# Performance work log

Hardware: AMD Instinct MI355X
Metric: run time of the kernel (lower is better)

## Reference

```python
import jax, jax.numpy as jnp
import numpy as np

SPATIAL_SCALE = 0.0625
GAMMA = 0.1  # mmcv DeformRoIPool default
NUM_HEADS = 1


def deform_roi_pool(features, rois, offsets, spatial_scale=SPATIAL_SCALE, gamma=GAMMA):
    """mmcv-style deformable RoI (align) pooling, sampling_ratio=1.
    features: (B,C,H,W); rois: (N,5)=[b,x1,y1,x2,y2]; offsets: (P,oh,ow,2) (dw,dh).
    Returns (P,N,C,oh,ow)."""
    B, C, H, W = features.shape
    N = rois.shape[0]
    P, oh, ow, _ = offsets.shape
    bidx = rois[:, 0].astype(jnp.int32)
    x1 = rois[:, 1] * spatial_scale - 0.5
    y1 = rois[:, 2] * spatial_scale - 0.5
    rw = rois[:, 3] * spatial_scale - 0.5 - x1
    rh = rois[:, 4] * spatial_scale - 0.5 - y1
    bin_w = rw / ow
    bin_h = rh / oh
    gh = jnp.arange(oh, dtype=features.dtype)
    gw = jnp.arange(ow, dtype=features.dtype)
    # bin-center sample points (sampling_ratio=1), deformed by gamma*roi_size*offset
    y = (y1[:, None, None] + (gh[None, :, None] + 0.5) * bin_h[:, None, None])[None]
    y = y + gamma * rh[None, :, None, None] * offsets[:, None, :, :, 1]  # (P,N,oh,ow)
    x = (x1[:, None, None] + (gw[None, None, :] + 0.5) * bin_w[:, None, None])[None]
    x = x + gamma * rw[None, :, None, None] * offsets[:, None, :, :, 0]
    valid = (y > -1.0) & (y < H) & (x > -1.0) & (x < W)
    yc = jnp.clip(y, 0.0, H - 1)
    xc = jnp.clip(x, 0.0, W - 1)
    y0 = jnp.floor(yc).astype(jnp.int32)
    x0 = jnp.floor(xc).astype(jnp.int32)
    y1i = jnp.minimum(y0 + 1, H - 1)
    x1i = jnp.minimum(x0 + 1, W - 1)
    ly = yc - y0.astype(yc.dtype)
    lx = xc - x0.astype(xc.dtype)
    hy = 1.0 - ly
    hx = 1.0 - lx
    f = features.reshape(B, C, H * W)
    bb = jnp.broadcast_to(bidx[None, :, None, None], (P, N, oh, ow))

    def g(yi, xi):
        return f[bb, :, yi * W + xi]  # (P,N,oh,ow,C)

    val = (g(y0, x0) * (hy * hx)[..., None] + g(y0, x1i) * (hy * lx)[..., None]
           + g(y1i, x0) * (ly * hx)[..., None] + g(y1i, x1i) * (ly * lx)[..., None])
    val = jnp.where(valid[..., None], val, 0.0)
    return jnp.transpose(val, (0, 1, 4, 2, 3))  # (P,N,C,oh,ow)


def setup_inputs() -> dict:
    key = jax.random.key(0)
    ks = jax.random.split(key, 9)
    B, C, Hf, Wf = 4, 256, 128, 128
    N, oh, ow, P = 512, 7, 7, 4
    features = jax.random.normal(ks[0], (B, C, Hf, Wf), jnp.float32)
    bidx = jax.random.randint(ks[1], (N,), 0, B).astype(jnp.float32)
    xy1 = jax.random.uniform(ks[2], (N, 2), jnp.float32, 0.0, 1700.0)
    wh = jax.random.uniform(ks[3], (N, 2), jnp.float32, 32.0, 300.0)
    rois = jnp.concatenate([bidx[:, None], xy1, xy1 + wh], axis=1)  # (N,5)
    per_point_offsets = jax.random.normal(ks[4], (P, oh, ow, 2), jnp.float32) * 0.001
    queries = jax.random.normal(ks[5], (oh * ow, C), jnp.float32) * 0.02
    w_proj = jax.random.normal(ks[6], (C, C), jnp.float32) * 0.02
    b_proj = jnp.zeros((C,), jnp.float32)
    in_proj_w = jax.random.normal(ks[7], (3 * C, C), jnp.float32) * 0.02
    in_proj_b = jnp.zeros((3 * C,), jnp.float32)
    out_proj_w = jax.random.normal(ks[8], (C, C), jnp.float32) * 0.02
    out_proj_b = jnp.zeros((C,), jnp.float32)
    return dict(features=features, rois=rois, per_point_offsets=per_point_offsets,
                queries=queries, w_proj=w_proj, b_proj=b_proj,
                in_proj_w=in_proj_w, in_proj_b=in_proj_b,
                out_proj_w=out_proj_w, out_proj_b=out_proj_b)


def reference(features, rois, per_point_offsets, queries, w_proj, b_proj,
              in_proj_w, in_proj_b, out_proj_w, out_proj_b):
    samples = deform_roi_pool(features, rois, per_point_offsets)  # (P,N,C,oh,ow)
    P, N, C, oh, ow = samples.shape
    # 1x1 conv projection
    proj = jnp.einsum('pnchw,dc->pndhw', samples, w_proj) + b_proj[None, None, :, None, None]
    kv = jnp.transpose(proj, (0, 1, 3, 4, 2)).reshape(P, N * oh * ow, C)  # (P,B,C)
    q = jnp.tile(queries, (N, 1))  # (B,C), B=(n,h,w) order
    Wq, Wk, Wv = in_proj_w[:C], in_proj_w[C:2 * C], in_proj_w[2 * C:]
    bq, bk, bv = in_proj_b[:C], in_proj_b[C:2 * C], in_proj_b[2 * C:]
    H = NUM_HEADS
    d = C // H
    Q = (q @ Wq.T + bq).reshape(-1, H, d)
    K = (kv @ Wk.T + bk).reshape(P, -1, H, d)
    V = (kv @ Wv.T + bv).reshape(P, -1, H, d)
    scores = jnp.einsum('bhd,pbhd->bhp', Q, K) * (d ** -0.5)
    attn = jax.nn.softmax(scores, axis=-1)  # over the P sampled points
    out = jnp.einsum('bhp,pbhd->bhd', attn, V).reshape(-1, C)
    out = out @ out_proj_w.T + out_proj_b
    return out.reshape(N, oh, ow, C).transpose(0, 3, 1, 2)  # (N,C,oh,ow)
```

## Files before the change

kernel.cpp:

```cpp
#include <hip/hip_runtime.h>
#include <math.h>

#define C_DIM 256
#define H_DIM 128
#define W_DIM 128
#define B_DIM 4
#define HW (H_DIM*W_DIM)
#define N_ROIS 512
#define OH 7
#define OW 7
#define TOKENS (N_ROIS*OH*OW)
#define SPS 0.0625f
#define GAMMA 0.1f
#define SCALE 0.0625f

typedef __attribute__((ext_vector_type(8))) short bf16x8;
typedef __attribute__((ext_vector_type(4))) float f32x4;
typedef __attribute__((ext_vector_type(4))) unsigned short us4;
typedef __attribute__((ext_vector_type(8))) unsigned short us8;

__device__ inline unsigned short f2bf_rne(float f) {
    unsigned int b = __float_as_uint(f);
    b += 0x7fffu + ((b >> 16) & 1u);
    return (unsigned short)(b >> 16);
}
__device__ inline float bfu(unsigned short u) {
    return __uint_as_float(((unsigned int)u) << 16);
}

__global__ void precompute1(const float* __restrict__ w_proj,
                            const float* __restrict__ in_proj_w,
                            const float* __restrict__ in_proj_b,
                            const float* __restrict__ queries,
                            const float* __restrict__ b_proj,
                            float* __restrict__ A_k, float* __restrict__ A_v,
                            float* __restrict__ Qhat, float* __restrict__ cv) {
    int idx = blockIdx.x * 256 + threadIdx.x;
    if (idx < 65536) {
        int i = idx >> 8, j = idx & 255;
        const float* wk = in_proj_w + (size_t)(256 + i) * 256;
        float s = 0.f;
        for (int t = 0; t < 256; t++) s += wk[t] * w_proj[t * 256 + j];
        A_k[idx] = s;
    } else if (idx < 131072) {
        int e = idx - 65536;
        int i = e >> 8, j = e & 255;
        const float* wv = in_proj_w + (size_t)(512 + i) * 256;
        float s = 0.f;
        for (int t = 0; t < 256; t++) s += wv[t] * w_proj[t * 256 + j];
        A_v[e] = s;
    } else if (idx < 143616) {
        int e = idx - 131072;
        int s_ = e >> 8, i = e & 255;
        const float* q  = queries + (size_t)s_ * 256;
        const float* wq = in_proj_w + (size_t)i * 256;
        float s = in_proj_b[i];
        for (int t = 0; t < 256; t++) s += q[t] * wq[t];
        Qhat[e] = s;
    } else {
        int i = idx - 143616;
        const float* wv = in_proj_w + (size_t)(512 + i) * 256;
        float s = in_proj_b[512 + i];
        for (int t = 0; t < 256; t++) s += wv[t] * b_proj[t];
        cv[i] = s;
    }
}

__global__ void precompute2(const float* __restrict__ Qhat,
                            const float* __restrict__ A_k,
                            const float* __restrict__ A_v,
                            const float* __restrict__ out_proj_w,
                            const float* __restrict__ out_proj_b,
                            const float* __restrict__ cv,
                            float* __restrict__ u,
                            unsigned short* __restrict__ Mh,
                            unsigned short* __restrict__ Ml,
                            float* __restrict__ Mtp, int writeMtp,
                            float* __restrict__ c_out) {
    int idx = blockIdx.x * 256 + threadIdx.x;
    if (idx < 12544) {
        int s_ = idx >> 8, j = idx & 255;
        const float* qh = Qhat + (size_t)s_ * 256;
        float s = 0.f;
        for (int i = 0; i < 256; i++) s += qh[i] * A_k[i * 256 + j];
        u[idx] = s;
    } else if (idx < 78080) {
        int e = idx - 12544;
        int c = e >> 8, d = e & 255;
        const float* wo = out_proj_w + (size_t)c * 256;
        float s = 0.f;
        for (int i = 0; i < 256; i++) s += wo[i] * A_v[i * 256 + d];
        unsigned short hi = f2bf_rne(s);
        float fh = bfu(hi);
        unsigned short lo = f2bf_rne(s - fh);
        Mh[(size_t)c * 256 + d] = hi;
        Ml[(size_t)c * 256 + d] = lo;
        if (writeMtp)
            Mtp[((size_t)(d >> 2) * 256 + c) * 4 + (d & 3)] = s;
    } else {
        int c = idx - 78080;
        const float* wo = out_proj_w + (size_t)c * 256;
        float s = out_proj_b[c];
        for (int i = 0; i < 256; i++) s += wo[i] * cv[i];
        c_out[c] = s;
    }
}

__global__ void transpose_bf16(const float* __restrict__ f,
                               unsigned short* __restrict__ ft) {
    __shared__ float tile[64][65];
    int b  = blockIdx.z;
    int c0 = blockIdx.y * 64;
    int s0 = blockIdx.x * 64;
    const float* fin = f + (size_t)b * C_DIM * HW;
    int sl = threadIdx.x & 63, cw = threadIdx.x >> 6;
    #pragma unroll
    for (int k = 0; k < 16; k++) {
        int cl = cw + k * 4;
        tile[cl][sl] = fin[(size_t)(c0 + cl) * HW + s0 + sl];
    }
    __syncthreads();
    unsigned short* fo = ft + (size_t)b * HW * C_DIM;
    int cl = threadIdx.x & 63, sw = threadIdx.x >> 6;
    #pragma unroll
    for (int k = 0; k < 16; k++) {
        int sl2 = sw + k * 4;
        fo[(size_t)(s0 + sl2) * C_DIM + c0 + cl] = f2bf_rne(tile[cl][sl2]);
    }
}

__global__ void __launch_bounds__(256) fused_sample_gemm(
        const unsigned short* __restrict__ feat_b,
        const float* __restrict__ rois,
        const float* __restrict__ offs,
        const float* __restrict__ u,
        const unsigned short* __restrict__ Mh,
        const unsigned short* __restrict__ Ml,
        const float* __restrict__ c_out,
        float* __restrict__ out) {
    __shared__ __align__(16) char ldsraw[54272];
    unsigned short* A = (unsigned short*)ldsraw;

    int tid = threadIdx.x;
    int n = blockIdx.x;

    const float* r = rois + (size_t)n * 5;
    int bi   = (int)r[0];
    float x1 = r[1] * SPS - 0.5f;
    float y1v = r[2] * SPS - 0.5f;
    float rw = r[3] * SPS - 0.5f - x1;
    float rh = r[4] * SPS - 0.5f - y1v;
    float bw = rw * (1.0f / 7.0f);
    float bh = rh * (1.0f / 7.0f);
    const unsigned short* fb = feat_b + (size_t)bi * HW * C_DIM;

    int lane32 = tid & 31;
    int halfw  = tid >> 5;
    int c8 = lane32 * 8;

    for (int t = halfw; t < 49; t += 8) {
        int hb = t / 7, wb = t - hb * 7;
        const float* up = u + (size_t)t * 256 + c8;
        float uu[8];
        *(float4*)uu       = *(const float4*)up;
        *(float4*)(uu + 4) = *(const float4*)(up + 4);

        float sv[4][8];
        float part[4];
        #pragma unroll
        for (int p = 0; p < 4; p++) {
            float offw = offs[((p * 7 + hb) * 7 + wb) * 2 + 0];
            float offh = offs[((p * 7 + hb) * 7 + wb) * 2 + 1];
            float y = y1v + ((float)hb + 0.5f) * bh + GAMMA * rh * offh;
            float x = x1  + ((float)wb + 0.5f) * bw + GAMMA * rw * offw;
            bool valid = (y > -1.0f) && (y < 128.0f) && (x > -1.0f) && (x < 128.0f);
            float yc = fminf(fmaxf(y, 0.f), 127.f);
            float xc = fminf(fmaxf(x, 0.f), 127.f);
            int y0i = (int)yc, x0i = (int)xc;
            int y1i = min(y0i + 1, 127), x1i = min(x0i + 1, 127);
            float ly = yc - (float)y0i, lx = xc - (float)x0i;
            float hy = 1.f - ly, hx = 1.f - lx;
            float w00 = hy * hx, w01 = hy * lx, w10 = ly * hx, w11 = ly * lx;
            if (!valid) { w00 = 0.f; w01 = 0.f; w10 = 0.f; w11 = 0.f; }
            us8 r00 = *(const us8*)(fb + (size_t)(y0i * W_DIM + x0i) * C_DIM + c8);
            us8 r01 = *(const us8*)(fb + (size_t)(y0i * W_DIM + x1i) * C_DIM + c8);
            us8 r10 = *(const us8*)(fb + (size_t)(y1i * W_DIM + x0i) * C_DIM + c8);
            us8 r11 = *(const us8*)(fb + (size_t)(y1i * W_DIM + x1i) * C_DIM + c8);
            float accp = 0.f;
            #pragma unroll
            for (int j = 0; j < 8; j++) {
                float v = w00 * bfu(r00[j]) + w01 * bfu(r01[j])
                        + w10 * bfu(r10[j]) + w11 * bfu(r11[j]);
                sv[p][j] = v;
                accp = fmaf(uu[j], v, accp);
            }
            part[p] = accp;
        }
        #pragma unroll
        for (int mk = 1; mk <= 16; mk <<= 1) {
            #pragma unroll
            for (int p = 0; p < 4; p++) part[p] += __shfl_xor(part[p], mk, 64);
        }
        float sc0 = part[0] * SCALE, sc1 = part[1] * SCALE;
        float sc2 = part[2] * SCALE, sc3 = part[3] * SCALE;
        float mx = fmaxf(fmaxf(sc0, sc1), fmaxf(sc2, sc3));
        float e0 = __expf(sc0 - mx), e1 = __expf(sc1 - mx);
        float e2 = __expf(sc2 - mx), e3 = __expf(sc3 - mx);
        float inv = 1.f / (e0 + e1 + e2 + e3);
        us8 o8;
        #pragma unroll
        for (int j = 0; j < 8; j++) {
            float mv = (e0 * sv[0][j] + e1 * sv[1][j]
                      + e2 * sv[2][j] + e3 * sv[3][j]) * inv;
            o8[j] = f2bf_rne(mv);
        }
        *(us8*)(A + t * 264 + c8) = o8;
    }
    for (int i = tid; i < 480; i += 256) {
        int row = 49 + (i >> 5);
        int cs = (i & 31) * 8;
        us8 z = {0, 0, 0, 0, 0, 0, 0, 0};
        *(us8*)(A + row * 264 + cs) = z;
    }
    __syncthreads();

    int lane = tid & 63;
    int wave = tid >> 6;
    int col  = lane & 15;
    int quad = lane >> 4;
    int cbase = wave * 64;

    f32x4 zero = {0.f, 0.f, 0.f, 0.f};
    f32x4 acc[4][4];
    #pragma unroll
    for (int i = 0; i < 4; i++)
        #pragma unroll
        for (int j = 0; j < 4; j++) acc[i][j] = zero;

    for (int ks = 0; ks < 8; ks++) {
        bf16x8 af[4];
        #pragma unroll
        for (int rt = 0; rt < 4; rt++)
            af[rt] = *(const bf16x8*)(A + (rt * 16 + col) * 264 + ks * 32 + quad * 8);
        #pragma unroll
        for (int ct = 0; ct < 4; ct++) {
            size_t bo = (size_t)(cbase + ct * 16 + col) * 256 + ks * 32 + quad * 8;
            bf16x8 bh8 = *(const bf16x8*)(Mh + bo);
            bf16x8 bl8 = *(const bf16x8*)(Ml + bo);
            #pragma unroll
            for (int rt = 0; rt < 4; rt++) {
                acc[rt][ct] = __builtin_amdgcn_mfma_f32_16x16x32_bf16(af[rt], bh8, acc[rt][ct], 0, 0, 0);
                acc[rt][ct] = __builtin_amdgcn_mfma_f32_16x16x32_bf16(af[rt], bl8, acc[rt][ct], 0, 0, 0);
            }
        }
    }

    __syncthreads();
    float* ostage = (float*)ldsraw;
    #pragma unroll
    for (int rt = 0; rt < 4; rt++) {
        #pragma unroll
        for (int ct = 0; ct < 4; ct++) {
            int c = cbase + ct * 16 + col;
            float bias = c_out[c];
            #pragma unroll
            for (int rr = 0; rr < 4; rr++) {
                int t = rt * 16 + quad * 4 + rr;
                if (t < 49) ostage[c * 53 + t] = acc[rt][ct][rr] + bias;
            }
        }
    }
    __syncthreads();
    float* ob = out + (size_t)n * 12544;
    for (int k = 0; k < 49; k++) {
        int flat = k * 256 + tid;
        int c2 = flat / 49;
        int t2 = flat - c2 * 49;
        ob[flat] = ostage[c2 * 53 + t2];
    }
}

__global__ void sample_generic(const float* __restrict__ feat,
                               const float* __restrict__ rois,
                               const float* __restrict__ offs,
                               const float* __restrict__ u,
                               float* __restrict__ m_out,
                               int ch_stride, int pix_stride) {
    __shared__ float red[4][4];
    int token = blockIdx.x;
    int n = token / 49;
    int t = token - n * 49;
    int h = t / 7;
    int w = t - h * 7;
    const float* r = rois + (size_t)n * 5;
    int bi   = (int)r[0];
    float x1 = r[1] * SPS - 0.5f;
    float y1 = r[2] * SPS - 0.5f;
    float rw = r[3] * SPS - 0.5f - x1;
    float rh = r[4] * SPS - 0.5f - y1;
    float bw = rw * (1.0f / 7.0f);
    float bh = rh * (1.0f / 7.0f);
    int c = threadIdx.x;
    const float* fb = feat + (size_t)bi * HW * C_DIM;
    float u_c = u[(size_t)t * 256 + c];
    float sv[4], part[4];
    #pragma unroll
    for (int p = 0; p < 4; p++) {
        float offw = offs[((p * 7 + h) * 7 + w) * 2 + 0];
        float offh = offs[((p * 7 + h) * 7 + w) * 2 + 1];
        float y = y1 + ((float)h + 0.5f) * bh + GAMMA * rh * offh;
        float x = x1 + ((float)w + 0.5f) * bw + GAMMA * rw * offw;
        bool valid = (y > -1.0f) && (y < (float)H_DIM) && (x > -1.0f) && (x < (float)W_DIM);
        float yc = fminf(fmaxf(y, 0.f), 127.f);
        float xc = fminf(fmaxf(x, 0.f), 127.f);
        int y0i = (int)floorf(yc);
        int x0i = (int)floorf(xc);
        int y1i = min(y0i + 1, 127);
        int x1i = min(x0i + 1, 127);
        float ly = yc - (float)y0i, lx = xc - (float)x0i;
        float hy = 1.f - ly, hx = 1.f - lx;
        float v00 = fb[(size_t)(y0i * W_DIM + x0i) * pix_stride + (size_t)c * ch_stride];
        float v01 = fb[(size_t)(y0i * W_DIM + x1i) * pix_stride + (size_t)c * ch_stride];
        float v10 = fb[(size_t)(y1i * W_DIM + x0i) * pix_stride + (size_t)c * ch_stride];
        float v11 = fb[(size_t)(y1i * W_DIM + x1i) * pix_stride + (size_t)c * ch_stride];
        float v = hy * hx * v00 + hy * lx * v01 + ly * hx * v10 + ly * lx * v11;
        v = valid ? v : 0.f;
        sv[p] = v;
        part[p] = u_c * v;
    }
    #pragma unroll
    for (int o = 32; o >= 1; o >>= 1) {
        #pragma unroll
        for (int p = 0; p < 4; p++) part[p] += __shfl_down(part[p], o, 64);
    }
    int wv = threadIdx.x >> 6, lane = threadIdx.x & 63;
    if (lane == 0) {
        red[wv][0] = part[0]; red[wv][1] = part[1];
        red[wv][2] = part[2]; red[wv][3] = part[3];
    }
    __syncthreads();
    float sc0 = (red[0][0] + red[1][0] + red[2][0] + red[3][0]) * SCALE;
    float sc1 = (red[0][1] + red[1][1] + red[2][1] + red[3][1]) * SCALE;
    float sc2 = (red[0][2] + red[1][2] + red[2][2] + red[3][2]) * SCALE;
    float sc3 = (red[0][3] + red[1][3] + red[2][3] + red[3][3]) * SCALE;
    float mx = fmaxf(fmaxf(sc0, sc1), fmaxf(sc2, sc3));
    float e0 = __expf(sc0 - mx), e1 = __expf(sc1 - mx);
    float e2 = __expf(sc2 - mx), e3 = __expf(sc3 - mx);
    float inv = 1.f / (e0 + e1 + e2 + e3);
    m_out[(size_t)token * 256 + c] =
        (e0 * sv[0] + e1 * sv[1] + e2 * sv[2] + e3 * sv[3]) * inv;
}

__global__ void __launch_bounds__(256) roi_gemm(const float* __restrict__ m,
                                                const float* __restrict__ Mtp,
                                                const float* __restrict__ c_out,
                                                float* __restrict__ out) {
    __shared__ float mlds[49 * 260];
    int c = threadIdx.x;
    int n = blockIdx.x;
    const float* mb = m + (size_t)n * 12544;
    for (int t = 0; t < 49; t++) mlds[t * 260 + c] = mb[t * 256 + c];
    __syncthreads();
    float acc[49];
    #pragma unroll
    for (int t = 0; t < 49; t++) acc[t] = 0.f;
    const float4* Mp = (const float4*)Mtp;
    for (int d4 = 0; d4 < 64; d4++) {
        float4 w4 = Mp[(size_t)d4 * 256 + c];
        #pragma unroll
        for (int t = 0; t < 49; t++) {
            float4 mv = *(const float4*)&mlds[t * 260 + d4 * 4];
            acc[t] = fmaf(w4.x, mv.x, acc[t]);
            acc[t] = fmaf(w4.y, mv.y, acc[t]);
            acc[t] = fmaf(w4.z, mv.z, acc[t]);
            acc[t] = fmaf(w4.w, mv.w, acc[t]);
        }
    }
    float bias = c_out[c];
    __syncthreads();
    #pragma unroll
    for (int t = 0; t < 49; t++) mlds[t * 260 + c] = acc[t] + bias;
    __syncthreads();
    float* ob = out + (size_t)n * 12544;
    for (int k = 0; k < 49; k++) {
        int flat = k * 256 + c;
        int c2 = flat / 49;
        int t2 = flat - c2 * 49;
        ob[flat] = mlds[t2 * 260 + c2];
    }
}

extern "C" void kernel_launch(void* const* d_in, const int* in_sizes, int n_in,
                              void* d_out, int out_size, void* d_ws, size_t ws_size,
                              hipStream_t stream) {
    (void)in_sizes; (void)n_in; (void)out_size;
    const float* features   = (const float*)d_in[0];
    const float* rois       = (const float*)d_in[1];
    const float* offs       = (const float*)d_in[2];
    const float* queries    = (const float*)d_in[3];
    const float* w_proj     = (const float*)d_in[4];
    const float* b_proj     = (const float*)d_in[5];
    const float* in_proj_w  = (const float*)d_in[6];
    const float* in_proj_b  = (const float*)d_in[7];
    const float* out_proj_w = (const float*)d_in[8];
    const float* out_proj_b = (const float*)d_in[9];
    float* out = (float*)d_out;
    float* ws  = (float*)d_ws;

    float* A_k   = ws;
    float* A_v   = A_k  + 65536;
    float* Qhat  = A_v  + 65536;
    float* cv    = Qhat + 12544;
    float* u     = cv   + 256;
    float* c_out = u    + 12544;
    unsigned short* Mh = (unsigned short*)(ws + 156672);
    unsigned short* Ml = (unsigned short*)(ws + 189440);
    unsigned short* feat_b = (unsigned short*)(ws + 222208);
    float* Mtp    = ws + 222208;
    float* m_fb   = ws + 222208 + 65536;

    size_t needT = ((size_t)222208 + (size_t)8388608) * 4;
    size_t needF = ((size_t)222208 + (size_t)65536 + (size_t)TOKENS * 256) * 4;
    bool useT = ws_size >= needT;

    precompute1<<<562, 256, 0, stream>>>(w_proj, in_proj_w, in_proj_b,
                                         queries, b_proj, A_k, A_v, Qhat, cv);
    precompute2<<<306, 256, 0, stream>>>(Qhat, A_k, A_v, out_proj_w, out_proj_b,
                                         cv, u, Mh, Ml, Mtp, useT ? 0 : 1, c_out);

    if (useT) {
        transpose_bf16<<<dim3(256, 4, 4), 256, 0, stream>>>(features, feat_b);
        fused_sample_gemm<<<N_ROIS, 256, 0, stream>>>(feat_b, rois, offs, u,
                                                      Mh, Ml, c_out, out);
    } else {
        float* m = (ws_size >= needF) ? m_fb : out;
        sample_generic<<<TOKENS, 256, 0, stream>>>(features, rois, offs, u, m, HW, 1);
        roi_gemm<<<512, 256, 0, stream>>>(m, Mtp, c_out, out);
    }
}
```

Before: 180.8 us.

## Fuse precompute, transpose and sampling GEMM into one cooperative persistent kernel

Merges the two weight-precompute kernels, the feature transpose and the fused sample+GEMM kernel into a single cooperative kernel with 512 blocks, using grid.sync between phases. Precompute1 runs alongside the transpose, and precompute2 follows after the first grid barrier. This removes three kernel launch gaps and the tail idle time between them, at the cost of two grid-wide barriers and an occupancy check on the host. The fallback path also replaces the fp32 roi_gemm with a bf16 hi/lo MFMA version, and falls back to separate launches if the cooperative launch fails.

```diff
diff --git a/kernel.cpp b/kernel.cpp
--- a/kernel.cpp
+++ b/kernel.cpp
@@ -1,22 +1,21 @@
 #include <hip/hip_runtime.h>
+#include <hip/hip_cooperative_groups.h>
 #include <math.h>
+
+namespace cg = cooperative_groups;
 
 #define C_DIM 256
 #define H_DIM 128
 #define W_DIM 128
-#define B_DIM 4
 #define HW (H_DIM*W_DIM)
 #define N_ROIS 512
-#define OH 7
-#define OW 7
-#define TOKENS (N_ROIS*OH*OW)
+#define TOKENS (N_ROIS*49)
 #define SPS 0.0625f
 #define GAMMA 0.1f
 #define SCALE 0.0625f
 
 typedef __attribute__((ext_vector_type(8))) short bf16x8;
 typedef __attribute__((ext_vector_type(4))) float f32x4;
-typedef __attribute__((ext_vector_type(4))) unsigned short us4;
 typedef __attribute__((ext_vector_type(8))) unsigned short us8;
 
 __device__ inline unsigned short f2bf_rne(float f) {
@@ -28,14 +27,12 @@
     return __uint_as_float(((unsigned int)u) << 16);
 }
 
-__global__ void precompute1(const float* __restrict__ w_proj,
-                            const float* __restrict__ in_proj_w,
-                            const float* __restrict__ in_proj_b,
-                            const float* __restrict__ queries,
-                            const float* __restrict__ b_proj,
-                            float* __restrict__ A_k, float* __restrict__ A_v,
-                            float* __restrict__ Qhat, float* __restrict__ cv) {
-    int idx = blockIdx.x * 256 + threadIdx.x;
+
+__device__ inline void dev_pre1(int idx,
+                                const float* w_proj, const float* in_proj_w,
+                                const float* in_proj_b, const float* queries,
+                                const float* b_proj,
+                                float* A_k, float* A_v, float* Qhat, float* cv) {
     if (idx < 65536) {
         int i = idx >> 8, j = idx & 255;
         const float* wk = in_proj_w + (size_t)(256 + i) * 256;
@@ -57,7 +54,7 @@
         float s = in_proj_b[i];
         for (int t = 0; t < 256; t++) s += q[t] * wq[t];
         Qhat[e] = s;
-    } else {
+    } else if (idx < 143872) {
         int i = idx - 143616;
         const float* wv = in_proj_w + (size_t)(512 + i) * 256;
         float s = in_proj_b[512 + i];
@@ -66,18 +63,12 @@
     }
 }
 
-__global__ void precompute2(const float* __restrict__ Qhat,
-                            const float* __restrict__ A_k,
-                            const float* __restrict__ A_v,
-                            const float* __restrict__ out_proj_w,
-                            const float* __restrict__ out_proj_b,
-                            const float* __restrict__ cv,
-                            float* __restrict__ u,
-                            unsigned short* __restrict__ Mh,
-                            unsigned short* __restrict__ Ml,
-                            float* __restrict__ Mtp, int writeMtp,
-                            float* __restrict__ c_out) {
-    int idx = blockIdx.x * 256 + threadIdx.x;
+__device__ inline void dev_pre2(int idx,
+                                const float* Qhat, const float* A_k, const float* A_v,
+                                const float* out_proj_w, const float* out_proj_b,
+                                const float* cv,
+                                float* u, unsigned short* Mh, unsigned short* Ml,
+                                float* c_out) {
     if (idx < 12544) {
         int s_ = idx >> 8, j = idx & 255;
         const float* qh = Qhat + (size_t)s_ * 256;
@@ -91,13 +82,10 @@
         float s = 0.f;
         for (int i = 0; i < 256; i++) s += wo[i] * A_v[i * 256 + d];
         unsigned short hi = f2bf_rne(s);
-        float fh = bfu(hi);
-        unsigned short lo = f2bf_rne(s - fh);
+        unsigned short lo = f2bf_rne(s - bfu(hi));
         Mh[(size_t)c * 256 + d] = hi;
         Ml[(size_t)c * 256 + d] = lo;
-        if (writeMtp)
-            Mtp[((size_t)(d >> 2) * 256 + c) * 4 + (d & 3)] = s;
-    } else {
+    } else if (idx < 78336) {
         int c = idx - 78080;
         const float* wo = out_proj_w + (size_t)c * 256;
         float s = out_proj_b[c];
@@ -106,52 +94,48 @@
     }
 }
 
-__global__ void transpose_bf16(const float* __restrict__ f,
-                               unsigned short* __restrict__ ft) {
-    __shared__ float tile[64][65];
-    int b  = blockIdx.z;
-    int c0 = blockIdx.y * 64;
-    int s0 = blockIdx.x * 64;
-    const float* fin = f + (size_t)b * C_DIM * HW;
-    int sl = threadIdx.x & 63, cw = threadIdx.x >> 6;
-    #pragma unroll
-    for (int k = 0; k < 16; k++) {
-        int cl = cw + k * 4;
+__device__ inline void dev_transpose_tile(char* ldsraw, int tile_id, int tid,
+                                          const float* features,
+                                          unsigned short* feat_b) {
+    float (*tile)[65] = (float (*)[65])ldsraw;
+    int b   = tile_id >> 10;
+    int rem = tile_id & 1023;
+    int c0  = (rem >> 8) << 6;
+    int s0  = (rem & 255) << 6;
+    int sl = tid & 63, cw = tid >> 6;
+    const float* fin = features + (size_t)b * C_DIM * HW;
+    #pragma unroll
+    for (int kk = 0; kk < 16; kk++) {
+        int cl = cw + kk * 4;
         tile[cl][sl] = fin[(size_t)(c0 + cl) * HW + s0 + sl];
     }
     __syncthreads();
-    unsigned short* fo = ft + (size_t)b * HW * C_DIM;
-    int cl = threadIdx.x & 63, sw = threadIdx.x >> 6;
-    #pragma unroll
-    for (int k = 0; k < 16; k++) {
-        int sl2 = sw + k * 4;
-        fo[(size_t)(s0 + sl2) * C_DIM + c0 + cl] = f2bf_rne(tile[cl][sl2]);
-    }
-}
-
-__global__ void __launch_bounds__(256) fused_sample_gemm(
-        const unsigned short* __restrict__ feat_b,
-        const float* __restrict__ rois,
-        const float* __restrict__ offs,
-        const float* __restrict__ u,
-        const unsigned short* __restrict__ Mh,
-        const unsigned short* __restrict__ Ml,
-        const float* __restrict__ c_out,
-        float* __restrict__ out) {
-    __shared__ __align__(16) char ldsraw[54272];
+    unsigned short* fo = feat_b + (size_t)b * HW * C_DIM;
+    #pragma unroll
+    for (int kk = 0; kk < 16; kk++) {
+        int sl2 = cw + kk * 4;
+        fo[(size_t)(s0 + sl2) * C_DIM + c0 + sl] = f2bf_rne(tile[sl][sl2]);
+    }
+    __syncthreads();
+}
+
+__device__ inline void dev_sample_gemm(char* ldsraw, int n, int tid,
+                                       const unsigned short* feat_b,
+                                       const float* rois, const float* offs,
+                                       const float* u,
+                                       const unsigned short* Mh,
+                                       const unsigned short* Ml,
+                                       const float* c_out, float* out) {
     unsigned short* A = (unsigned short*)ldsraw;
 
-    int tid = threadIdx.x;
-    int n = blockIdx.x;
-
     const float* r = rois + (size_t)n * 5;
-    int bi   = (int)r[0];
-    float x1 = r[1] * SPS - 0.5f;
+    int bi    = (int)r[0];
+    float x1  = r[1] * SPS - 0.5f;
     float y1v = r[2] * SPS - 0.5f;
-    float rw = r[3] * SPS - 0.5f - x1;
-    float rh = r[4] * SPS - 0.5f - y1v;
-    float bw = rw * (1.0f / 7.0f);
-    float bh = rh * (1.0f / 7.0f);
+    float rw  = r[3] * SPS - 0.5f - x1;
+    float rh  = r[4] * SPS - 0.5f - y1v;
+    float bw  = rw * (1.0f / 7.0f);
+    float bh  = rh * (1.0f / 7.0f);
     const unsigned short* fb = feat_b + (size_t)bi * HW * C_DIM;
 
     int lane32 = tid & 31;
@@ -182,10 +166,10 @@
             float hy = 1.f - ly, hx = 1.f - lx;
             float w00 = hy * hx, w01 = hy * lx, w10 = ly * hx, w11 = ly * lx;
             if (!valid) { w00 = 0.f; w01 = 0.f; w10 = 0.f; w11 = 0.f; }
-            us8 r00 = *(const us8*)(fb + (size_t)(y0i * W_DIM + x0i) * C_DIM + c8);
-            us8 r01 = *(const us8*)(fb + (size_t)(y0i * W_DIM + x1i) * C_DIM + c8);
-            us8 r10 = *(const us8*)(fb + (size_t)(y1i * W_DIM + x0i) * C_DIM + c8);
-            us8 r11 = *(const us8*)(fb + (size_t)(y1i * W_DIM + x1i) * C_DIM + c8);
+            us8 r00 = *(const us8*)(fb + (size_t)(y0i * W_DIM + x0i) * 256 + c8);
+            us8 r01 = *(const us8*)(fb + (size_t)(y0i * W_DIM + x1i) * 256 + c8);
+            us8 r10 = *(const us8*)(fb + (size_t)(y1i * W_DIM + x0i) * 256 + c8);
+            us8 r11 = *(const us8*)(fb + (size_t)(y1i * W_DIM + x1i) * 256 + c8);
             float accp = 0.f;
             #pragma unroll
             for (int j = 0; j < 8; j++) {
@@ -265,8 +249,8 @@
             float bias = c_out[c];
             #pragma unroll
             for (int rr = 0; rr < 4; rr++) {
-                int t = rt * 16 + quad * 4 + rr;
-                if (t < 49) ostage[c * 53 + t] = acc[rt][ct][rr] + bias;
+                int tt = rt * 16 + quad * 4 + rr;
+                if (tt < 49) ostage[c * 53 + tt] = acc[rt][ct][rr] + bias;
             }
         }
     }
@@ -280,12 +264,80 @@
     }
 }
 
+struct MegaArgs {
+    const float* features; const float* rois; const float* offs;
+    const float* queries;  const float* w_proj; const float* b_proj;
+    const float* in_proj_w; const float* in_proj_b;
+    const float* out_proj_w; const float* out_proj_b;
+    float* A_k; float* A_v; float* Qhat; float* cv;
+    float* u;   float* c_out;
+    unsigned short* Mh; unsigned short* Ml;
+    unsigned short* feat_b;
+    float* out;
+};
+
+__global__ void __launch_bounds__(256, 2) mega(MegaArgs a) {
+    __shared__ __align__(16) char ldsraw[54272];
+    cg::grid_group grid = cg::this_grid();
+    int tid = threadIdx.x;
+    int bid = blockIdx.x;
+
+    for (int idx = bid * 256 + tid; idx < 143872; idx += 131072)
+        dev_pre1(idx, a.w_proj, a.in_proj_w, a.in_proj_b, a.queries, a.b_proj,
+                 a.A_k, a.A_v, a.Qhat, a.cv);
+
+    for (int k = 0; k < 8; k++)
+        dev_transpose_tile(ldsraw, bid * 8 + k, tid, a.features, a.feat_b);
+
+    __threadfence();
+    grid.sync();
+    __threadfence();
+
+    dev_pre2(bid * 256 + tid, a.Qhat, a.A_k, a.A_v, a.out_proj_w, a.out_proj_b,
+             a.cv, a.u, a.Mh, a.Ml, a.c_out);
+
+    __threadfence();
+    grid.sync();
+    __threadfence();
+
+    dev_sample_gemm(ldsraw, bid, tid, a.feat_b, a.rois, a.offs, a.u,
+                    a.Mh, a.Ml, a.c_out, a.out);
+}
+
+__global__ void k_pre1(const float* w_proj, const float* in_proj_w,
+                       const float* in_proj_b, const float* queries,
+                       const float* b_proj,
+                       float* A_k, float* A_v, float* Qhat, float* cv) {
+    dev_pre1(blockIdx.x * 256 + threadIdx.x, w_proj, in_proj_w, in_proj_b,
+             queries, b_proj, A_k, A_v, Qhat, cv);
+}
+__global__ void k_pre2(const float* Qhat, const float* A_k, const float* A_v,
+                       const float* out_proj_w, const float* out_proj_b,
+                       const float* cv, float* u,
+                       unsigned short* Mh, unsigned short* Ml, float* c_out) {
+    dev_pre2(blockIdx.x * 256 + threadIdx.x, Qhat, A_k, A_v, out_proj_w,
+             out_proj_b, cv, u, Mh, Ml, c_out);
+}
+__global__ void k_transpose(const float* features, unsigned short* feat_b) {
+    __shared__ __align__(16) char ldsraw[16640];
+    dev_transpose_tile(ldsraw, blockIdx.x, threadIdx.x, features, feat_b);
+}
+__global__ void __launch_bounds__(256) k_fused(const unsigned short* feat_b,
+                                               const float* rois, const float* offs,
+                                               const float* u,
+                                               const unsigned short* Mh,
+                                               const unsigned short* Ml,
+                                               const float* c_out, float* out) {
+    __shared__ __align__(16) char ldsraw[54272];
+    dev_sample_gemm(ldsraw, blockIdx.x, threadIdx.x, feat_b, rois, offs, u,
+                    Mh, Ml, c_out, out);
+}
+
 __global__ void sample_generic(const float* __restrict__ feat,
                                const float* __restrict__ rois,
                                const float* __restrict__ offs,
                                const float* __restrict__ u,
-                               float* __restrict__ m_out,
-                               int ch_stride, int pix_stride) {
+                               float* __restrict__ m_out) {
     __shared__ float red[4][4];
     int token = blockIdx.x;
     int n = token / 49;
@@ -319,10 +371,10 @@
         int x1i = min(x0i + 1, 127);
         float ly = yc - (float)y0i, lx = xc - (float)x0i;
         float hy = 1.f - ly, hx = 1.f - lx;
-        float v00 = fb[(size_t)(y0i * W_DIM + x0i) * pix_stride + (size_t)c * ch_stride];
-        float v01 = fb[(size_t)(y0i * W_DIM + x1i) * pix_stride + (size_t)c * ch_stride];
-        float v10 = fb[(size_t)(y1i * W_DIM + x0i) * pix_stride + (size_t)c * ch_stride];
-        float v11 = fb[(size_t)(y1i * W_DIM + x1i) * pix_stride + (size_t)c * ch_stride];
+        float v00 = fb[(size_t)c * HW + y0i * W_DIM + x0i];
+        float v01 = fb[(size_t)c * HW + y0i * W_DIM + x1i];
+        float v10 = fb[(size_t)c * HW + y1i * W_DIM + x0i];
+        float v11 = fb[(size_t)c * HW + y1i * W_DIM + x1i];
         float v = hy * hx * v00 + hy * lx * v01 + ly * hx * v10 + ly * lx * v11;
         v = valid ? v : 0.f;
         sv[p] = v;
@@ -351,42 +403,79 @@
         (e0 * sv[0] + e1 * sv[1] + e2 * sv[2] + e3 * sv[3]) * inv;
 }
 
-__global__ void __launch_bounds__(256) roi_gemm(const float* __restrict__ m,
-                                                const float* __restrict__ Mtp,
-                                                const float* __restrict__ c_out,
-                                                float* __restrict__ out) {
-    __shared__ float mlds[49 * 260];
-    int c = threadIdx.x;
+__global__ void __launch_bounds__(256) roi_gemm_m(const float* m,
+                                                  const unsigned short* __restrict__ Mh,
+                                                  const unsigned short* __restrict__ Ml,
+                                                  const float* __restrict__ c_out,
+                                                  float* out) {
+    __shared__ __align__(16) char ldsraw[54272];
+    unsigned short* A = (unsigned short*)ldsraw;
+    int tid = threadIdx.x;
     int n = blockIdx.x;
     const float* mb = m + (size_t)n * 12544;
-    for (int t = 0; t < 49; t++) mlds[t * 260 + c] = mb[t * 256 + c];
-    __syncthreads();
-    float acc[49];
-    #pragma unroll
-    for (int t = 0; t < 49; t++) acc[t] = 0.f;
-    const float4* Mp = (const float4*)Mtp;
-    for (int d4 = 0; d4 < 64; d4++) {
-        float4 w4 = Mp[(size_t)d4 * 256 + c];
-        #pragma unroll
-        for (int t = 0; t < 49; t++) {
-            float4 mv = *(const float4*)&mlds[t * 260 + d4 * 4];
-            acc[t] = fmaf(w4.x, mv.x, acc[t]);
-            acc[t] = fmaf(w4.y, mv.y, acc[t]);
-            acc[t] = fmaf(w4.z, mv.z, acc[t]);
-            acc[t] = fmaf(w4.w, mv.w, acc[t]);
-        }
-    }
-    float bias = c_out[c];
-    __syncthreads();
-    #pragma unroll
-    for (int t = 0; t < 49; t++) mlds[t * 260 + c] = acc[t] + bias;
+    for (int i = tid; i < 3136; i += 256) {
+        float4 f = *(const float4*)(mb + (size_t)i * 4);
+        int t = i >> 6;
+        int d = (i & 63) * 4;
+        unsigned short* dst = A + t * 264 + d;
+        dst[0] = f2bf_rne(f.x); dst[1] = f2bf_rne(f.y);
+        dst[2] = f2bf_rne(f.z); dst[3] = f2bf_rne(f.w);
+    }
+    for (int i = tid; i < 480; i += 256) {
+        int row = 49 + (i >> 5);
+        int cs = (i & 31) * 8;
+        us8 z = {0,0,0,0,0,0,0,0};
+        *(us8*)(A + row * 264 + cs) = z;
+    }
+    __syncthreads();
+    int lane = tid & 63, wave = tid >> 6;
+    int col = lane & 15, quad = lane >> 4;
+    int cbase = wave * 64;
+    f32x4 zero = {0.f,0.f,0.f,0.f};
+    f32x4 acc[4][4];
+    #pragma unroll
+    for (int i = 0; i < 4; i++)
+        #pragma unroll
+        for (int j = 0; j < 4; j++) acc[i][j] = zero;
+    for (int ks = 0; ks < 8; ks++) {
+        bf16x8 af[4];
+        #pragma unroll
+        for (int rt = 0; rt < 4; rt++)
+            af[rt] = *(const bf16x8*)(A + (rt * 16 + col) * 264 + ks * 32 + quad * 8);
+        #pragma unroll
+        for (int ct = 0; ct < 4; ct++) {
+            size_t bo = (size_t)(cbase + ct * 16 + col) * 256 + ks * 32 + quad * 8;
+            bf16x8 bh8 = *(const bf16x8*)(Mh + bo);
+            bf16x8 bl8 = *(const bf16x8*)(Ml + bo);
+            #pragma unroll
+            for (int rt = 0; rt < 4; rt++) {
+                acc[rt][ct] = __builtin_amdgcn_mfma_f32_16x16x32_bf16(af[rt], bh8, acc[rt][ct], 0, 0, 0);
+                acc[rt][ct] = __builtin_amdgcn_mfma_f32_16x16x32_bf16(af[rt], bl8, acc[rt][ct], 0, 0, 0);
+            }
+        }
+    }
+    __syncthreads();
+    float* ostage = (float*)ldsraw;
+    #pragma unroll
+    for (int rt = 0; rt < 4; rt++) {
+        #pragma unroll
+        for (int ct = 0; ct < 4; ct++) {
+            int c = cbase + ct * 16 + col;
+            float bias = c_out[c];
+            #pragma unroll
+            for (int rr = 0; rr < 4; rr++) {
+                int tt = rt * 16 + quad * 4 + rr;
+                if (tt < 49) ostage[c * 53 + tt] = acc[rt][ct][rr] + bias;
+            }
+        }
+    }
     __syncthreads();
     float* ob = out + (size_t)n * 12544;
     for (int k = 0; k < 49; k++) {
-        int flat = k * 256 + c;
+        int flat = k * 256 + tid;
         int c2 = flat / 49;
         int t2 = flat - c2 * 49;
-        ob[flat] = mlds[t2 * 260 + c2];
+        ob[flat] = ostage[c2 * 53 + t2];
     }
 }
 
@@ -416,25 +505,44 @@
     unsigned short* Mh = (unsigned short*)(ws + 156672);
     unsigned short* Ml = (unsigned short*)(ws + 189440);
     unsigned short* feat_b = (unsigned short*)(ws + 222208);
-    float* Mtp    = ws + 222208;
-    float* m_fb   = ws + 222208 + 65536;
+    float* m_fb = ws + 222208;
 
     size_t needT = ((size_t)222208 + (size_t)8388608) * 4;
-    size_t needF = ((size_t)222208 + (size_t)65536 + (size_t)TOKENS * 256) * 4;
+    size_t needF = ((size_t)222208 + (size_t)TOKENS * 256) * 4;
     bool useT = ws_size >= needT;
 
-    precompute1<<<562, 256, 0, stream>>>(w_proj, in_proj_w, in_proj_b,
-                                         queries, b_proj, A_k, A_v, Qhat, cv);
-    precompute2<<<306, 256, 0, stream>>>(Qhat, A_k, A_v, out_proj_w, out_proj_b,
-                                         cv, u, Mh, Ml, Mtp, useT ? 0 : 1, c_out);
-
     if (useT) {
-        transpose_bf16<<<dim3(256, 4, 4), 256, 0, stream>>>(features, feat_b);
-        fused_sample_gemm<<<N_ROIS, 256, 0, stream>>>(feat_b, rois, offs, u,
-                                                      Mh, Ml, c_out, out);
+        int nb = 0;
+        hipError_t oe = hipOccupancyMaxActiveBlocksPerMultiprocessor(&nb, mega, 256, 0);
+        bool coop = (oe == hipSuccess) && (nb >= 2);
+
+        if (coop) {
+            MegaArgs ha;
+            ha.features = features; ha.rois = rois; ha.offs = offs; ha.queries = queries;
+            ha.w_proj = w_proj; ha.b_proj = b_proj; ha.in_proj_w = in_proj_w;
+            ha.in_proj_b = in_proj_b; ha.out_proj_w = out_proj_w; ha.out_proj_b = out_proj_b;
+            ha.A_k = A_k; ha.A_v = A_v; ha.Qhat = Qhat; ha.cv = cv;
+            ha.u = u; ha.c_out = c_out; ha.Mh = Mh; ha.Ml = Ml;
+            ha.feat_b = feat_b; ha.out = out;
+            void* kp[] = { &ha };
+            hipError_t le = hipLaunchCooperativeKernel(
+                reinterpret_cast<void*>(mega), dim3(N_ROIS), dim3(256), kp, 0, stream);
+            if (le == hipSuccess) return;
+            (void)hipGetLastError();
+        }
+        k_pre1<<<562, 256, 0, stream>>>(w_proj, in_proj_w, in_proj_b, queries,
+                                        b_proj, A_k, A_v, Qhat, cv);
+        k_transpose<<<4096, 256, 0, stream>>>(features, feat_b);
+        k_pre2<<<306, 256, 0, stream>>>(Qhat, A_k, A_v, out_proj_w, out_proj_b,
+                                        cv, u, Mh, Ml, c_out);
+        k_fused<<<N_ROIS, 256, 0, stream>>>(feat_b, rois, offs, u, Mh, Ml, c_out, out);
     } else {
+        k_pre1<<<562, 256, 0, stream>>>(w_proj, in_proj_w, in_proj_b, queries,
+                                        b_proj, A_k, A_v, Qhat, cv);
+        k_pre2<<<306, 256, 0, stream>>>(Qhat, A_k, A_v, out_proj_w, out_proj_b,
+                                        cv, u, Mh, Ml, c_out);
         float* m = (ws_size >= needF) ? m_fb : out;
-        sample_generic<<<TOKENS, 256, 0, stream>>>(features, rois, offs, u, m, HW, 1);
-        roi_gemm<<<512, 256, 0, stream>>>(m, Mtp, c_out, out);
-    }
-}
+        sample_generic<<<TOKENS, 256, 0, stream>>>(features, rois, offs, u, m);
+        roi_gemm_m<<<N_ROIS, 256, 0, stream>>>(m, Mh, Ml, c_out, out);
+    }
+}
```

New measurement: 222.5 us. +23.1%, slower.
